# Optimization experiments

Measured on AMD Instinct MI355X. Metric: run time of the kernel, lower is better.

The kernel has to match this reference:

```python
import jax, jax.numpy as jnp
import numpy as np

SIZE = 128      # reconstruction grid (size x size)
ANGLES = 128    # number of projection angles after interpolation
B, C, H, W = 2, 8, 128, 128  # batch, channels, detector rows (z-slices), detector cols
N_VIEWS = 8


def setup_inputs() -> dict:
    key = jax.random.key(0)
    keys = jax.random.split(key, N_VIEWS)
    return {f"f{i}": jax.random.normal(keys[i], (B, C, H, W), dtype=jnp.float32)
            for i in range(N_VIEWS)}


def _fbp(projections, size, n_angles):
    # projections: (B, C, H, V, W) -- V stacked views, W detector columns
    b, c, h, v, w = projections.shape
    # Interpolation step: resize V views -> n_angles angles (linear, half-pixel,
    # matching F.interpolate default semantics)
    sino = jax.image.resize(projections, (b, c, h, n_angles, w), method="linear")
    # Ram-Lak ramp filter along the detector-column axis
    ramp = jnp.abs(jnp.fft.fftfreq(w)).astype(jnp.float32)
    filt = jnp.real(jnp.fft.ifft(jnp.fft.fft(sino, axis=-1) * ramp, axis=-1)).astype(sino.dtype)
    # Back-projection (parallel beam, per z-slice H)
    thetas = jnp.arange(n_angles, dtype=jnp.float32) * (jnp.pi / n_angles)
    xs = jnp.arange(size, dtype=jnp.float32) - (size - 1) / 2.0
    X, Y = jnp.meshgrid(xs, xs, indexing="xy")  # (S, S)
    center = (w - 1) / 2.0

    sino_per_angle = jnp.moveaxis(filt, 3, 0)  # (A, B, C, H, W)

    def body(acc, inputs):
        theta, sino_a = inputs                       # sino_a: (B, C, H, W)
        t = X * jnp.cos(theta) + Y * jnp.sin(theta) + center  # (S, S)
        t = jnp.clip(t, 0.0, w - 1.0)
        t0 = jnp.floor(t).astype(jnp.int32)
        t1 = jnp.minimum(t0 + 1, w - 1)
        w1 = (t - t0).astype(sino_a.dtype)
        v0 = sino_a[..., t0]                         # (B, C, H, S, S) gather
        v1 = sino_a[..., t1]
        acc = acc + v0 * (1.0 - w1) + v1 * w1
        return acc, None

    acc0 = jnp.zeros((b, c, h, size, size), dtype=sino.dtype)
    vol, _ = jax.lax.scan(body, acc0, (thetas, sino_per_angle))
    return vol * (jnp.pi / (2.0 * n_angles))


def reference(f0, f1, f2, f3, f4, f5, f6, f7):
    # torch.cat([f.unsqueeze(3) for f in features], dim=3) == stack on new axis 3
    projections = jnp.stack([f0, f1, f2, f3, f4, f5, f6, f7], axis=3)  # (B,C,H,V,W)
    return _fbp(projections, SIZE, ANGLES)
```

## Files before the change

### kernel.cpp

```cpp
#include <hip/hip_runtime.h>
#include <math.h>

#define W 128
#define NANG 128
#define SZ 128
#define NV 8
#define NROWS 2048
#define K_DIM 1024
#define NPIX 16384
#define OUT_SCALE 0.012271846303085130f

typedef _Float16 f16x8 __attribute__((ext_vector_type(8)));
typedef float    f32x4 __attribute__((ext_vector_type(4)));


struct Ptrs8 { const float* p[8]; };

__device__ __forceinline__ void glds16(const void* g, void* l) {
    __builtin_amdgcn_global_load_lds(
        (const __attribute__((address_space(1))) void*)g,
        (__attribute__((address_space(3))) void*)l, 16, 0, 0);
}

__global__ void k_tables(float* __restrict__ kt, float2* __restrict__ cs) {
    int d = threadIdx.x;
    const float w0 = 6.283185307179586f / (float)W * (float)d;
    float s = 0.f;
    for (int f = 1; f < 64; ++f)
        s = fmaf((float)f, __cosf(w0 * (float)f), s);
    s = 2.f * s + 64.f * ((d & 1) ? -1.f : 1.f);
    kt[d] = s * (1.f / (float)(W * W));
    float th = (float)d * ((float)M_PI / (float)NANG);
    cs[d] = make_float2(cosf(th), sinf(th));
}

__global__ void k_filter(Ptrs8 in, const float* __restrict__ kt,
                         _Float16* __restrict__ pf) {
    int blk = blockIdx.x;
    int r = blk >> 3, v = blk & 7;
    __shared__ float row[W];
    __shared__ float kk[W];
    int n = threadIdx.x;
    row[n] = in.p[v][r * W + n];
    kk[n]  = kt[n];
    __syncthreads();
    float s = 0.f;
#pragma unroll 8
    for (int m = 0; m < W; ++m)
        s = fmaf(row[m], kk[(n - m) & (W - 1)], s);
    pf[(size_t)r * K_DIM + v * W + n] = (_Float16)s;
}

__global__ void k_wv(const float2* __restrict__ cs, _Float16* __restrict__ wv) {
    __shared__ float wrow[8 * K_DIM];
    const int tid = threadIdx.x;
    const int p0 = blockIdx.x * 8;
    for (int i = tid; i < 8 * K_DIM; i += 256) wrow[i] = 0.f;
    __syncthreads();
    const int px  = tid >> 5;
    const int sub = tid & 31;
    const int p = p0 + px;
    const float x = (float)(p & 127) - 63.5f;
    const float y = (float)(p >> 7) - 63.5f;
    float* prow = &wrow[px * K_DIM];
    for (int a = sub; a < NANG; a += 32) {
        float2 c = cs[a];
        float t = fmaf(x, c.x, fmaf(y, c.y, 63.5f));
        t = fminf(fmaxf(t, 0.f), 127.f);
        float tf = fminf(floorf(t), 126.f);
        int   ti = (int)tf;
        float wt = t - tf;
        float src = ((float)a + 0.5f) * 0.0625f - 0.5f;
        src = fminf(fmaxf(src, 0.f), 7.f);
        float vf = floorf(src);
        int   v0 = (int)vf;
        int   v1 = v0 + 1 < NV ? v0 + 1 : NV - 1;
        float wa = src - vf;
        float wA0 = (1.f - wa) * OUT_SCALE;
        atomicAdd(&prow[v0 * W + ti],     wA0 * (1.f - wt));
        atomicAdd(&prow[v0 * W + ti + 1], wA0 * wt);
        if (v1 != v0) {
            float wA1 = wa * OUT_SCALE;
            atomicAdd(&prow[v1 * W + ti],     wA1 * (1.f - wt));
            atomicAdd(&prow[v1 * W + ti + 1], wA1 * wt);
        }
    }
    __syncthreads();
    for (int i = tid; i < 8 * K_DIM; i += 256) {
        int pp = i >> 10, kk2 = i & 1023;
        wv[(size_t)(p0 + pp) * K_DIM + kk2] = (_Float16)wrow[i];
    }
}

__global__ __launch_bounds__(256)
void k_gemm(const _Float16* __restrict__ A,
            const _Float16* __restrict__ B,
            float* __restrict__ out) {
    __shared__ _Float16 sA[128 * 32];
    __shared__ _Float16 sB[128 * 32];
    const int tid  = threadIdx.x;
    const int lane = tid & 63, wave = tid >> 6;
    const int m0 = blockIdx.y * 128;
    const int n0 = blockIdx.x * 128;
    const int wm = wave >> 1, wn = wave & 1;

    f32x4 acc[4][4] = {};

    const int c0 = wave * 64 + lane;
    const int c1 = c0 + 256;
    const _Float16* gA0 = A + (size_t)(m0 + (c0 >> 2)) * K_DIM + (c0 & 3) * 8;
    const _Float16* gA1 = A + (size_t)(m0 + (c1 >> 2)) * K_DIM + (c1 & 3) * 8;
    const _Float16* gB0 = B + (size_t)(n0 + (c0 >> 2)) * K_DIM + (c0 & 3) * 8;
    const _Float16* gB1 = B + (size_t)(n0 + (c1 >> 2)) * K_DIM + (c1 & 3) * 8;
    _Float16* lA0 = sA + wave * 512;
    _Float16* lA1 = sA + 2048 + wave * 512;
    _Float16* lB0 = sB + wave * 512;
    _Float16* lB1 = sB + 2048 + wave * 512;

    const int fr = lane & 15;
    const int fg = lane >> 4;

    for (int kb = 0; kb < K_DIM; kb += 32) {
        glds16(gA0 + kb, lA0);
        glds16(gA1 + kb, lA1);
        glds16(gB0 + kb, lB0);
        glds16(gB1 + kb, lB1);
        __syncthreads();
        f16x8 af[4], bf[4];
#pragma unroll
        for (int mt = 0; mt < 4; ++mt)
            af[mt] = *(const f16x8*)&sA[((wm * 4 + mt) * 16 + fr) * 32 + fg * 8];
#pragma unroll
        for (int nt = 0; nt < 4; ++nt)
            bf[nt] = *(const f16x8*)&sB[((wn * 4 + nt) * 16 + fr) * 32 + fg * 8];
#pragma unroll
        for (int mt = 0; mt < 4; ++mt)
#pragma unroll
            for (int nt = 0; nt < 4; ++nt)
                acc[mt][nt] = __builtin_amdgcn_mfma_f32_16x16x32_f16(
                    af[mt], bf[nt], acc[mt][nt], 0, 0, 0);
        __syncthreads();
    }

#pragma unroll
    for (int mt = 0; mt < 4; ++mt) {
#pragma unroll
        for (int nt = 0; nt < 4; ++nt) {
            int m = m0 + (wm * 4 + mt) * 16 + fg * 4;
            int n = n0 + (wn * 4 + nt) * 16 + fr;
            float* op = out + (size_t)m * NPIX + n;
#pragma unroll
            for (int rr = 0; rr < 4; ++rr)
                op[(size_t)rr * NPIX] = acc[mt][nt][rr];
        }
    }
}

extern "C" void kernel_launch(void* const* d_in, const int* in_sizes, int n_in,
                              void* d_out, int out_size, void* d_ws, size_t ws_size,
                              hipStream_t stream) {
    float*      kt = (float*)d_ws;
    float2*     cs = (float2*)((char*)d_ws + 512);
    _Float16*   pf = (_Float16*)((char*)d_ws + 4096);
    _Float16*   wv = (_Float16*)((char*)d_ws + 4096 + (size_t)NROWS * K_DIM * 2);

    Ptrs8 in;
    for (int i = 0; i < NV; ++i) in.p[i] = (const float*)d_in[i];

    k_tables<<<1, 128, 0, stream>>>(kt, cs);
    k_filter<<<NROWS * NV, 128, 0, stream>>>(in, kt, pf);
    k_wv<<<NPIX / 8, 256, 0, stream>>>(cs, wv);
    dim3 grid(NPIX / 128, NROWS / 128);
    k_gemm<<<grid, 256, 0, stream>>>(pf, wv, (float*)d_out);
}
```

Before: 314.0 us.

## Recast ramp filter as circulant-matrix MFMA GEMM and vectorize wv stores

The scalar per-row circular convolution kernel is replaced by an fp16 MFMA GEMM. Each block loads 64 detector rows, converted to half precision, and multiplies them by a 128x128 circulant filter matrix that k_tables precomputes into the workspace. This is meant to cut the many tiny launches and scalar FMA loops of the old filter stage. It also packs the k_wv fp16 output into 32-bit stores. The inputs are now rounded to fp16 before filtering rather than after, which adds some precision loss.

```diff
diff --git a/kernel.cpp b/kernel.cpp
--- a/kernel.cpp
+++ b/kernel.cpp
@@ -11,8 +11,12 @@
 #define OUT_SCALE 0.012271846303085130f
 
 typedef _Float16 f16x8 __attribute__((ext_vector_type(8)));
+typedef _Float16 f16x4 __attribute__((ext_vector_type(4)));
 typedef float    f32x4 __attribute__((ext_vector_type(4)));
 
+#define CF_OFF 4096
+#define PF_OFF 36864
+#define WV_OFF (36864 + (size_t)NROWS * K_DIM * 2)
 
 struct Ptrs8 { const float* p[8]; };
 
@@ -22,33 +26,72 @@
         (__attribute__((address_space(3))) void*)l, 16, 0, 0);
 }
 
-__global__ void k_tables(float* __restrict__ kt, float2* __restrict__ cs) {
+__global__ void k_tables(float* __restrict__ kt, float2* __restrict__ cs,
+                         _Float16* __restrict__ cf) {
+    __shared__ float kl[W];
     int d = threadIdx.x;
     const float w0 = 6.283185307179586f / (float)W * (float)d;
     float s = 0.f;
     for (int f = 1; f < 64; ++f)
         s = fmaf((float)f, __cosf(w0 * (float)f), s);
     s = 2.f * s + 64.f * ((d & 1) ? -1.f : 1.f);
-    kt[d] = s * (1.f / (float)(W * W));
+    float kv = s * (1.f / (float)(W * W));
+    kt[d] = kv;
+    kl[d] = kv;
     float th = (float)d * ((float)M_PI / (float)NANG);
     cs[d] = make_float2(cosf(th), sinf(th));
-}
-
-__global__ void k_filter(Ptrs8 in, const float* __restrict__ kt,
-                         _Float16* __restrict__ pf) {
-    int blk = blockIdx.x;
-    int r = blk >> 3, v = blk & 7;
-    __shared__ float row[W];
-    __shared__ float kk[W];
-    int n = threadIdx.x;
-    row[n] = in.p[v][r * W + n];
-    kk[n]  = kt[n];
-    __syncthreads();
-    float s = 0.f;
-#pragma unroll 8
-    for (int m = 0; m < W; ++m)
-        s = fmaf(row[m], kk[(n - m) & (W - 1)], s);
-    pf[(size_t)r * K_DIM + v * W + n] = (_Float16)s;
+    __syncthreads();
+    for (int k = 0; k < W; ++k)
+        cf[d * W + k] = (_Float16)kl[(d - k) & (W - 1)];
+}
+
+#define FS_A 136
+__global__ __launch_bounds__(256)
+void k_fgemm(Ptrs8 in, const _Float16* __restrict__ cf,
+             _Float16* __restrict__ pf) {
+    __shared__ _Float16 sA[64 * FS_A];
+    __shared__ _Float16 sB[128 * FS_A];
+    const int tid  = threadIdx.x;
+    const int lane = tid & 63, wave = tid >> 6;
+    const int fr = lane & 15, fg = lane >> 4;
+    const int blk = blockIdx.x;
+
+    {
+        const int i   = tid >> 5;
+        const int pos = (tid & 31) * 4;
+#pragma unroll
+        for (int v = 0; v < NV; ++v) {
+            float4 x = *(const float4*)(in.p[v] + (size_t)(blk * 8 + i) * W + pos);
+            f16x4 h = { (_Float16)x.x, (_Float16)x.y, (_Float16)x.z, (_Float16)x.w };
+            *(f16x4*)&sA[(i * 8 + v) * FS_A + pos] = h;
+        }
+    }
+#pragma unroll
+    for (int j = 0; j < 8; ++j) {
+        int c = tid + 256 * j;
+        int n = c >> 4, kp = (c & 15) * 8;
+        *(f16x8*)&sB[n * FS_A + kp] = *(const f16x8*)&cf[n * W + kp];
+    }
+    __syncthreads();
+
+    f32x4 acc[8] = {};
+#pragma unroll
+    for (int kb = 0; kb < W; kb += 32) {
+        f16x8 af = *(const f16x8*)&sA[(wave * 16 + fr) * FS_A + kb + fg * 8];
+#pragma unroll
+        for (int nt = 0; nt < 8; ++nt) {
+            f16x8 bf = *(const f16x8*)&sB[(nt * 16 + fr) * FS_A + kb + fg * 8];
+            acc[nt] = __builtin_amdgcn_mfma_f32_16x16x32_f16(af, bf, acc[nt], 0, 0, 0);
+        }
+    }
+#pragma unroll
+    for (int nt = 0; nt < 8; ++nt) {
+        int m = blk * 64 + wave * 16 + fg * 4;
+        int n = nt * 16 + fr;
+#pragma unroll
+        for (int rr = 0; rr < 4; ++rr)
+            pf[(size_t)(m + rr) * W + n] = (_Float16)acc[nt][rr];
+    }
 }
 
 __global__ void k_wv(const float2* __restrict__ cs, _Float16* __restrict__ wv) {
@@ -86,9 +129,14 @@
         }
     }
     __syncthreads();
-    for (int i = tid; i < 8 * K_DIM; i += 256) {
-        int pp = i >> 10, kk2 = i & 1023;
-        wv[(size_t)(p0 + pp) * K_DIM + kk2] = (_Float16)wrow[i];
+    uint* wvu = (uint*)(wv + (size_t)p0 * K_DIM);
+#pragma unroll
+    for (int j = 0; j < 16; ++j) {
+        int j2 = tid + 256 * j;
+        float2 w2 = *(const float2*)&wrow[j2 * 2];
+        union { uint u; struct { _Float16 lo, hi; } h; } pk;
+        pk.h.lo = (_Float16)w2.x; pk.h.hi = (_Float16)w2.y;
+        wvu[j2] = pk.u;
     }
 }
 
@@ -161,14 +209,15 @@
                               hipStream_t stream) {
     float*      kt = (float*)d_ws;
     float2*     cs = (float2*)((char*)d_ws + 512);
-    _Float16*   pf = (_Float16*)((char*)d_ws + 4096);
-    _Float16*   wv = (_Float16*)((char*)d_ws + 4096 + (size_t)NROWS * K_DIM * 2);
+    _Float16*   cf = (_Float16*)((char*)d_ws + CF_OFF);
+    _Float16*   pf = (_Float16*)((char*)d_ws + PF_OFF);
+    _Float16*   wv = (_Float16*)((char*)d_ws + WV_OFF);
 
     Ptrs8 in;
     for (int i = 0; i < NV; ++i) in.p[i] = (const float*)d_in[i];
 
-    k_tables<<<1, 128, 0, stream>>>(kt, cs);
-    k_filter<<<NROWS * NV, 128, 0, stream>>>(in, kt, pf);
+    k_tables<<<1, 128, 0, stream>>>(kt, cs, cf);
+    k_fgemm<<<NROWS * NV / 64, 256, 0, stream>>>(in, cf, pf);
     k_wv<<<NPIX / 8, 256, 0, stream>>>(cs, wv);
     dim3 grid(NPIX / 128, NROWS / 128);
     k_gemm<<<grid, 256, 0, stream>>>(pf, wv, (float*)d_out);
```

Result: faster. 294.6 us (-6.2%).
